# Kernel optimization log

Measured on AMD Instinct MI355X. Metric: run time of the kernel, lower is better.

Reference implementation:

```python
import jax, jax.numpy as jnp
import numpy as np

B, S, H = 8, 2048, 512
M = 4096
TEMP = 0.1
EPS = 1e-6


def setup_inputs() -> dict:
    key = jax.random.key(0)
    ks = jax.random.split(key, 8)
    scale = 1.0 / np.sqrt(H)
    return {
        "hidden_states": jax.random.normal(ks[0], (B, S, H), dtype=jnp.float32),
        "memory_keys": jax.random.normal(ks[1], (M, H), dtype=jnp.float32),
        "memory_values": jax.random.normal(ks[2], (M, H), dtype=jnp.float32),
        "Wk": jax.random.normal(ks[3], (H, H), dtype=jnp.float32) * scale,
        "bk": jnp.zeros((H,), dtype=jnp.float32),
        "Wo": jax.random.normal(ks[4], (H, H), dtype=jnp.float32) * scale,
        "bo": jnp.zeros((H,), dtype=jnp.float32),
        "memory_usage": jax.random.randint(ks[5], (M,), 0, 2, dtype=jnp.int32),
    }


def reference(hidden_states, memory_keys, memory_values, Wk, bk, Wo, bo, memory_usage):
    # key projection: [B,S,H]
    q = jnp.einsum("bsh,kh->bsk", hidden_states, Wk) + bk
    # L2-style normalization with eps inside rsqrt (matches torch.rsqrt(norm_sq + 1e-6))
    q_n = q * jax.lax.rsqrt(jnp.sum(q * q, axis=-1, keepdims=True) + EPS)
    mk_n = memory_keys * jax.lax.rsqrt(
        jnp.sum(memory_keys * memory_keys, axis=-1, keepdims=True) + EPS
    )
    # cosine-similarity scores over the memory bank: [B,S,M]
    scores = jnp.einsum("bsk,mk->bsm", q_n, mk_n) / TEMP
    mask = (memory_usage > 0).astype(scores.dtype)  # [M]
    scores = scores * mask + (-1e9) * (1.0 - mask)
    attn = jax.nn.softmax(scores, axis=-1)  # [B,S,M]
    retrieved = jnp.einsum("bsm,mv->bsv", attn, memory_values)  # [B,S,H]
    out = jnp.einsum("bsv,hv->bsh", retrieved, Wo) + bo
    return out
```

## Files before the change

kernel.cpp:

```cpp
#include <hip/hip_runtime.h>
#include <cstdint>
#include <cstddef>

#define H_DIM   512
#define M_DIM   4096

typedef unsigned short u16;
typedef short bf16x8 __attribute__((ext_vector_type(8)));
typedef float f32x4  __attribute__((ext_vector_type(4)));

__device__ __forceinline__ u16 f2b(float f) {
  union { float f; uint32_t u; } v; v.f = f;
  uint32_t u = v.u + (0x7FFFu + ((v.u >> 16) & 1u));
  return (u16)(u >> 16);
}

__global__ void k_f2bf(const float* __restrict__ in, u16* __restrict__ out, int n4) {
  int i = blockIdx.x * blockDim.x + threadIdx.x;
  if (i < n4) {
    float4 v = ((const float4*)in)[i];
    ushort4 o;
    o.x = f2b(v.x); o.y = f2b(v.y); o.z = f2b(v.z); o.w = f2b(v.w);
    ((ushort4*)out)[i] = o;
  }
}

__global__ void k_f2bf_ww(const float* __restrict__ wk, const float* __restrict__ wo,
                          u16* __restrict__ owk, u16* __restrict__ owo) {
  int i = blockIdx.x * blockDim.x + threadIdx.x;
  const float* src = (i < 65536) ? wk : wo;
  u16* dst = (i < 65536) ? owk : owo;
  int j = i & 65535;
  float4 v = ((const float4*)src)[j];
  ushort4 o;
  o.x = f2b(v.x); o.y = f2b(v.y); o.z = f2b(v.z); o.w = f2b(v.w);
  ((ushort4*)dst)[j] = o;
}

__global__ void k_compact(const int* __restrict__ usage, int* __restrict__ idx,
                          int* __restrict__ meta) {
  __shared__ int cnt[256];
  int t = threadIdx.x;
  int base = t * 16;
  int c = 0;
  #pragma unroll
  for (int i = 0; i < 16; ++i) c += (usage[base + i] > 0) ? 1 : 0;
  cnt[t] = c;
  __syncthreads();
  for (int d = 1; d < 256; d <<= 1) {
    int v = (t >= d) ? cnt[t - d] : 0;
    __syncthreads();
    cnt[t] += v;
    __syncthreads();
  }
  int pos = cnt[t] - c;
  for (int i = 0; i < 16; ++i)
    if (usage[base + i] > 0) idx[pos++] = base + i;
  if (t == 0) {
    int total = cnt[255];
    int keff = ((total + 127) >> 7) << 7;
    meta[0] = total; meta[1] = keff; meta[2] = keff >> 5; meta[3] = keff >> 7;
  }
}

__global__ void k_gather_both(const float* __restrict__ keys, const float* __restrict__ vals,
                              const int* __restrict__ idx, const int* __restrict__ meta,
                              u16* __restrict__ okeys, u16* __restrict__ ovals) {
  int j    = blockIdx.x * 4 + (threadIdx.x >> 6);
  int lane = threadIdx.x & 63;
  int count = meta[0];
  ushort4* kp = (ushort4*)(okeys + (size_t)j * H_DIM);
  ushort4* vp = (ushort4*)(ovals + (size_t)j * H_DIM);
  if (j >= count) {
    ushort4 z = {0, 0, 0, 0};
    kp[lane] = z; kp[lane + 64] = z;
    vp[lane] = z; vp[lane + 64] = z;
    return;
  }
  int src = idx[j];
  const float4* rp = (const float4*)(keys + (size_t)src * H_DIM);
  float4 a = rp[lane];
  float4 b = rp[lane + 64];
  float ss = a.x*a.x + a.y*a.y + a.z*a.z + a.w*a.w
           + b.x*b.x + b.y*b.y + b.z*b.z + b.w*b.w;
  #pragma unroll
  for (int d = 1; d < 64; d <<= 1) ss += __shfl_xor(ss, d, 64);
  float s = rsqrtf(ss + 1e-6f);
  ushort4 oa, ob;
  oa.x = f2b(a.x*s); oa.y = f2b(a.y*s); oa.z = f2b(a.z*s); oa.w = f2b(a.w*s);
  ob.x = f2b(b.x*s); ob.y = f2b(b.y*s); ob.z = f2b(b.z*s); ob.w = f2b(b.w*s);
  kp[lane]      = oa;
  kp[lane + 64] = ob;
  const float4* vr = (const float4*)(vals + (size_t)src * H_DIM);
  float4 c0 = vr[lane];
  float4 c1 = vr[lane + 64];
  ushort4 va, vb;
  va.x = f2b(c0.x); va.y = f2b(c0.y); va.z = f2b(c0.z); va.w = f2b(c0.w);
  vb.x = f2b(c1.x); vb.y = f2b(c1.y); vb.z = f2b(c1.z); vb.w = f2b(c1.w);
  vp[lane]      = va;
  vp[lane + 64] = vb;
}

__global__ void k_rsq(const float* __restrict__ qss, float* __restrict__ rsq) {
  int r = blockIdx.x * blockDim.x + threadIdx.x;
  float s = 0.0f;
  #pragma unroll
  for (int i = 0; i < 8; ++i) s += qss[(size_t)r * 8 + i];
  rsq[r] = rsqrtf(s + 1e-6f);
}

__global__ void k_reduce_l(const float* __restrict__ lpart, float* __restrict__ linv,
                           const int* __restrict__ meta) {
  int r = blockIdx.x * blockDim.x + threadIdx.x;
  int n = meta[1] >> 6;
  float s = 0.0f;
  for (int i = 0; i < n; ++i) s += lpart[(size_t)r * 64 + i];
  linv[r] = 1.0f / s;
}

#define EPI_QPROJ 0
#define EPI_MW    1
#define EPI_P     2
#define EPI_OUT   3

template<int EPI>
__global__ __launch_bounds__(256, 3)
void k_gemm_bt(const u16* __restrict__ A, const u16* __restrict__ B,
               int N, int K,
               const int* __restrict__ meta,
               float* __restrict__ outf, u16* __restrict__ outh,
               const float* __restrict__ bias,
               float* __restrict__ aux,
               const float* __restrict__ rowscale) {
  __shared__ u16 Ah[2][128 * 32];
  __shared__ u16 Bh[2][128 * 32];

  const int tid  = threadIdx.x;
  const int wave = tid >> 6, lane = tid & 63;
  const int wr = (wave >> 1) * 64;
  const int wc = (wave & 1) * 64;

  int t0, t_end, t_step, kel, fixedb;
  if (EPI == EPI_QPROJ) {
    fixedb = blockIdx.x; t0 = blockIdx.y; t_end = t0 + 1; t_step = 1; kel = K;
  } else if (EPI == EPI_MW) {
    fixedb = blockIdx.y; t0 = blockIdx.x; t_end = meta[1] >> 7; t_step = 16; kel = K;
  } else if (EPI == EPI_P) {
    int id = blockIdx.x + (blockIdx.y << 4);
    int xcd = id & 7, s = id >> 3;
    fixedb = xcd * 16 + (s >> 4);
    t0 = s & 15;
    t_end = meta[1] >> 7; t_step = 16; kel = K;
  } else {
    int id = blockIdx.x + (blockIdx.y << 2);
    int xcd = id & 7, s = id >> 3;
    fixedb = xcd * 16 + (s >> 2);
    t0 = s & 3; t_end = t0 + 1; t_step = 1; kel = meta[1];
  }
  const int kiters = kel >> 5;

  const int srow   = lane & 15;
  const int schunk = lane >> 4;
  const int lds_off = schunk * 128 + srow * 8;

  const int fr = lane & 15;
  const int fbase = (lane >> 4) * 128 + fr * 8;
  const int g = lane >> 4;

  const char* Ac = (const char*)A;
  const char* Bc = (const char*)B;

  for (int t = t0; t < t_end; t += t_step) {
    const int row0 = ((EPI == EPI_P) ? t : fixedb) << 7;
    const int col0 = ((EPI == EPI_P) ? fixedb : t) << 7;
    __syncthreads();

    uint32_t aB[2], bB[2];
    #pragma unroll
    for (int s2 = 0; s2 < 2; ++s2) {
      aB[s2] = (uint32_t)(((size_t)(row0 + (wave + s2 * 4) * 16 + srow) * (size_t)K
                           + (size_t)(schunk * 8)) * 2u);
      bB[s2] = (uint32_t)(((size_t)(col0 + (wave + s2 * 4) * 16 + srow) * (size_t)K
                           + (size_t)(schunk * 8)) * 2u);
    }

    f32x4 acc[4][4];
    const f32x4 z = {0.0f, 0.0f, 0.0f, 0.0f};
    #pragma unroll
    for (int i = 0; i < 4; ++i)
      #pragma unroll
      for (int j = 0; j < 4; ++j) acc[i][j] = z;

    bf16x8 rA[2], rB[2];
    auto gload = [&](int k0) {
      const uint32_t kb = (uint32_t)(k0 << 1);
      #pragma unroll
      for (int s2 = 0; s2 < 2; ++s2) rA[s2] = *(const bf16x8*)(Ac + aB[s2] + kb);
      #pragma unroll
      for (int s2 = 0; s2 < 2; ++s2) rB[s2] = *(const bf16x8*)(Bc + bB[s2] + kb);
    };

    gload(0);
    for (int it = 0; it < kiters; ++it) {
      const int cur = it & 1;
      #pragma unroll
      for (int s2 = 0; s2 < 2; ++s2)
        *(bf16x8*)&Ah[cur][(wave + s2 * 4) * 512 + lds_off] = rA[s2];
      #pragma unroll
      for (int s2 = 0; s2 < 2; ++s2)
        *(bf16x8*)&Bh[cur][(wave + s2 * 4) * 512 + lds_off] = rB[s2];
      if (it + 1 < kiters) gload((it + 1) << 5);
      __syncthreads();

      bf16x8 af[4], bfv[4];
      #pragma unroll
      for (int i = 0; i < 4; ++i)
        af[i] = *(const bf16x8*)&Ah[cur][((wr >> 4) + i) * 512 + fbase];
      #pragma unroll
      for (int j = 0; j < 4; ++j)
        bfv[j] = *(const bf16x8*)&Bh[cur][((wc >> 4) + j) * 512 + fbase];
      #pragma unroll
      for (int i = 0; i < 4; ++i)
        #pragma unroll
        for (int j = 0; j < 4; ++j)
          acc[i][j] = __builtin_amdgcn_mfma_f32_16x16x32_bf16(af[i], bfv[j], acc[i][j], 0, 0, 0);
    }

    if (EPI == EPI_QPROJ) {
      float sj[4] = {0.f, 0.f, 0.f, 0.f};
      #pragma unroll
      for (int i = 0; i < 4; ++i) {
        const int kb = row0 + wr + i * 16 + g * 4;
        const float4 bkv = *(const float4*)(bias + kb);
        #pragma unroll
        for (int j = 0; j < 4; ++j) {
          const size_t rcol = (size_t)(col0 + wc + j * 16 + fr);
          float v0 = acc[i][j][0] + bkv.x;
          float v1 = acc[i][j][1] + bkv.y;
          float v2 = acc[i][j][2] + bkv.z;
          float v3 = acc[i][j][3] + bkv.w;
          ushort4 st; st.x = f2b(v0); st.y = f2b(v1); st.z = f2b(v2); st.w = f2b(v3);
          *(ushort4*)(outh + rcol * H_DIM + kb) = st;
          sj[j] += v0 * v0 + v1 * v1 + v2 * v2 + v3 * v3;
        }
      }
      const int slot = (row0 + wr) >> 6;
      #pragma unroll
      for (int j = 0; j < 4; ++j) {
        float s = sj[j];
        s += __shfl_xor(s, 16, 64);
        s += __shfl_xor(s, 32, 64);
        if (lane < 16)
          aux[(size_t)(col0 + wc + j * 16 + lane) * 8 + slot] = s;
      }
    } else if (EPI == EPI_MW) {
      #pragma unroll
      for (int i = 0; i < 4; ++i) {
        #pragma unroll
        for (int r = 0; r < 4; ++r) {
          int grow = row0 + wr + i * 16 + g * 4 + r;
          #pragma unroll
          for (int j = 0; j < 4; ++j) {
            int gcol = col0 + wc + j * 16 + fr;
            outh[(size_t)grow * (size_t)N + gcol] = f2b(acc[i][j][r]);
          }
        }
      }
    } else if (EPI == EPI_P) {
      const int count = meta[0];
      float rq10[4];
      #pragma unroll
      for (int j = 0; j < 4; ++j)
        rq10[j] = rowscale[col0 + wc + j * 16 + fr] * 10.0f;
      float sj[4] = {0.f, 0.f, 0.f, 0.f};
      #pragma unroll
      for (int i = 0; i < 4; ++i) {
        const int mb = row0 + wr + i * 16 + g * 4;
        #pragma unroll
        for (int j = 0; j < 4; ++j) {
          const size_t rcol = (size_t)(col0 + wc + j * 16 + fr);
          float p0 = (mb + 0 < count) ? __expf(acc[i][j][0] * rq10[j]) : 0.0f;
          float p1 = (mb + 1 < count) ? __expf(acc[i][j][1] * rq10[j]) : 0.0f;
          float p2 = (mb + 2 < count) ? __expf(acc[i][j][2] * rq10[j]) : 0.0f;
          float p3 = (mb + 3 < count) ? __expf(acc[i][j][3] * rq10[j]) : 0.0f;
          ushort4 st; st.x = f2b(p0); st.y = f2b(p1); st.z = f2b(p2); st.w = f2b(p3);
          *(ushort4*)(outh + rcol * M_DIM + mb) = st;
          sj[j] += (p0 + p1) + (p2 + p3);
        }
      }
      const int slot = (row0 + wr) >> 6;
      #pragma unroll
      for (int j = 0; j < 4; ++j) {
        float s = sj[j];
        s += __shfl_xor(s, 16, 64);
        s += __shfl_xor(s, 32, 64);
        if (lane < 16)
          aux[(size_t)(col0 + wc + j * 16 + lane) * 64 + slot] = s;
      }
    } else {
      float bv[4];
      #pragma unroll
      for (int j = 0; j < 4; ++j) bv[j] = bias[col0 + wc + j * 16 + fr];
      #pragma unroll
      for (int i = 0; i < 4; ++i) {
        #pragma unroll
        for (int r = 0; r < 4; ++r) {
          int grow = row0 + wr + i * 16 + g * 4 + r;
          float sc = rowscale[grow];
          #pragma unroll
          for (int j = 0; j < 4; ++j) {
            int gcol = col0 + wc + j * 16 + fr;
            outf[(size_t)grow * (size_t)N + gcol] = acc[i][j][r] * sc + bv[j];
          }
        }
      }
    }
  }
}

extern "C" void kernel_launch(void* const* d_in, const int* in_sizes, int n_in,
                              void* d_out, int out_size, void* d_ws, size_t ws_size,
                              hipStream_t stream) {
  const float* hidden = (const float*)d_in[0];
  const float* mkeys  = (const float*)d_in[1];
  const float* mvals  = (const float*)d_in[2];
  const float* Wk     = (const float*)d_in[3];
  const float* bk     = (const float*)d_in[4];
  const float* Wo     = (const float*)d_in[5];
  const float* bo     = (const float*)d_in[6];
  const int*   usage  = (const int*)d_in[7];
  (void)in_sizes; (void)n_in; (void)out_size; (void)ws_size;

  char* ws = (char*)d_ws;
  u16*   hb    = (u16*)(ws + 0);
  int*   idx   = (int*)(ws + 0);
  int*   meta  = (int*)(ws + 16384);
  float* lpart = (float*)(ws + 1048576);
  u16*   wkb   = (u16*)(ws + 16777216);
  u16*   wob   = (u16*)(ws + 17301504);
  u16*   mkn   = (u16*)(ws + 17825792);
  u16*   mv_c  = (u16*)(ws + 22020096);
  u16*   qb    = (u16*)(ws + 26214400);
  u16*   MWt   = (u16*)(ws + 42991616);
  u16*   P     = (u16*)(ws + 47185920);
  float* qss   = (float*)(ws + 47185920);
  float* rsqQ  = (float*)(ws + 181665792);
  float* linv  = (float*)(ws + 183828480);

  k_f2bf<<<8192, 256, 0, stream>>>(hidden, hb, 2097152);
  k_f2bf_ww<<<512, 256, 0, stream>>>(Wk, Wo, wkb, wob);

  k_gemm_bt<EPI_QPROJ><<<dim3(4, 128), 256, 0, stream>>>(wkb, hb, 512, 512,
      nullptr, nullptr, qb, bk, qss, nullptr);
  k_rsq<<<64, 256, 0, stream>>>(qss, rsqQ);

  k_compact<<<1, 256, 0, stream>>>(usage, idx, meta);
  k_gather_both<<<1024, 256, 0, stream>>>(mkeys, mvals, idx, meta, mkn, mv_c);

  k_gemm_bt<EPI_MW><<<dim3(16, 4), 256, 0, stream>>>(wob, mv_c, M_DIM, 512,
      meta, nullptr, MWt, nullptr, nullptr, nullptr);

  k_gemm_bt<EPI_P><<<dim3(16, 128), 256, 0, stream>>>(mkn, qb, M_DIM, 512,
      meta, nullptr, P, nullptr, lpart, rsqQ);
  k_reduce_l<<<64, 256, 0, stream>>>(lpart, linv, meta);

  k_gemm_bt<EPI_OUT><<<dim3(4, 128), 256, 0, stream>>>(P, MWt, 512, M_DIM,
      meta, (float*)d_out, nullptr, bo, nullptr, linv);
}
```

Measured before the change: 292.4 us.

## Use larger 256-wide tiles with 512-thread blocks for the two big GEMMs

Adds a new GEMM kernel with 512-thread blocks and 256x256 (scores) or 128x256 (output) tiles, and uses it for the score/exp GEMM and the final output GEMM. Each tile reuses operands more per LDS load and needs fewer blocks. The output GEMM swaps operand roles so it writes float4 rows with a vectorized bias add. The score kernel exits early on tiles beyond the compacted memory count and zeros the adjacent partial-sum slot. Larger tiles raise register and LDS use per block and may lower occupancy.

```diff
diff --git a/kernel.cpp b/kernel.cpp
--- a/kernel.cpp
+++ b/kernel.cpp
@@ -120,8 +120,6 @@
 
 #define EPI_QPROJ 0
 #define EPI_MW    1
-#define EPI_P     2
-#define EPI_OUT   3
 
 template<int EPI>
 __global__ __launch_bounds__(256, 3)
@@ -143,19 +141,8 @@
   int t0, t_end, t_step, kel, fixedb;
   if (EPI == EPI_QPROJ) {
     fixedb = blockIdx.x; t0 = blockIdx.y; t_end = t0 + 1; t_step = 1; kel = K;
-  } else if (EPI == EPI_MW) {
+  } else {
     fixedb = blockIdx.y; t0 = blockIdx.x; t_end = meta[1] >> 7; t_step = 16; kel = K;
-  } else if (EPI == EPI_P) {
-    int id = blockIdx.x + (blockIdx.y << 4);
-    int xcd = id & 7, s = id >> 3;
-    fixedb = xcd * 16 + (s >> 4);
-    t0 = s & 15;
-    t_end = meta[1] >> 7; t_step = 16; kel = K;
-  } else {
-    int id = blockIdx.x + (blockIdx.y << 2);
-    int xcd = id & 7, s = id >> 3;
-    fixedb = xcd * 16 + (s >> 2);
-    t0 = s & 3; t_end = t0 + 1; t_step = 1; kel = meta[1];
   }
   const int kiters = kel >> 5;
 
@@ -171,8 +158,8 @@
   const char* Bc = (const char*)B;
 
   for (int t = t0; t < t_end; t += t_step) {
-    const int row0 = ((EPI == EPI_P) ? t : fixedb) << 7;
-    const int col0 = ((EPI == EPI_P) ? fixedb : t) << 7;
+    const int row0 = fixedb << 7;
+    const int col0 = t << 7;
     __syncthreads();
 
     uint32_t aB[2], bB[2];
@@ -253,7 +240,7 @@
         if (lane < 16)
           aux[(size_t)(col0 + wc + j * 16 + lane) * 8 + slot] = s;
       }
-    } else if (EPI == EPI_MW) {
+    } else {
       #pragma unroll
       for (int i = 0; i < 4; ++i) {
         #pragma unroll
@@ -266,53 +253,168 @@
           }
         }
       }
-    } else if (EPI == EPI_P) {
-      const int count = meta[0];
-      float rq10[4];
-      #pragma unroll
-      for (int j = 0; j < 4; ++j)
-        rq10[j] = rowscale[col0 + wc + j * 16 + fr] * 10.0f;
-      float sj[4] = {0.f, 0.f, 0.f, 0.f};
-      #pragma unroll
-      for (int i = 0; i < 4; ++i) {
-        const int mb = row0 + wr + i * 16 + g * 4;
-        #pragma unroll
-        for (int j = 0; j < 4; ++j) {
-          const size_t rcol = (size_t)(col0 + wc + j * 16 + fr);
-          float p0 = (mb + 0 < count) ? __expf(acc[i][j][0] * rq10[j]) : 0.0f;
-          float p1 = (mb + 1 < count) ? __expf(acc[i][j][1] * rq10[j]) : 0.0f;
-          float p2 = (mb + 2 < count) ? __expf(acc[i][j][2] * rq10[j]) : 0.0f;
-          float p3 = (mb + 3 < count) ? __expf(acc[i][j][3] * rq10[j]) : 0.0f;
-          ushort4 st; st.x = f2b(p0); st.y = f2b(p1); st.z = f2b(p2); st.w = f2b(p3);
-          *(ushort4*)(outh + rcol * M_DIM + mb) = st;
-          sj[j] += (p0 + p1) + (p2 + p3);
-        }
-      }
-      const int slot = (row0 + wr) >> 6;
-      #pragma unroll
-      for (int j = 0; j < 4; ++j) {
-        float s = sj[j];
-        s += __shfl_xor(s, 16, 64);
-        s += __shfl_xor(s, 32, 64);
-        if (lane < 16)
-          aux[(size_t)(col0 + wc + j * 16 + lane) * 64 + slot] = s;
-      }
-    } else {
-      float bv[4];
-      #pragma unroll
-      for (int j = 0; j < 4; ++j) bv[j] = bias[col0 + wc + j * 16 + fr];
-      #pragma unroll
-      for (int i = 0; i < 4; ++i) {
-        #pragma unroll
-        for (int r = 0; r < 4; ++r) {
-          int grow = row0 + wr + i * 16 + g * 4 + r;
-          float sc = rowscale[grow];
-          #pragma unroll
-          for (int j = 0; j < 4; ++j) {
-            int gcol = col0 + wc + j * 16 + fr;
-            outf[(size_t)grow * (size_t)N + gcol] = acc[i][j][r] * sc + bv[j];
-          }
-        }
+    }
+  }
+}
+
+#define EPI2_P   0
+#define EPI2_OUT 1
+
+template<int EPI>
+__global__ __launch_bounds__(512, 2)
+void k_gemm2(const u16* __restrict__ A, const u16* __restrict__ B,
+             const int* __restrict__ meta,
+             float* __restrict__ outf, u16* __restrict__ outh,
+             const float* __restrict__ bias,
+             float* __restrict__ aux,
+             const float* __restrict__ rowscale) {
+  constexpr int BM  = (EPI == EPI2_P) ? 256 : 128;
+  constexpr int MF  = BM / 32;
+  constexpr int NF  = 4;
+  constexpr int NLA = BM / 128;
+  constexpr int NLB = 2;
+
+  __shared__ u16 Ah[2][BM * 32];
+  __shared__ u16 Bh[2][256 * 32];
+
+  const int tid  = threadIdx.x;
+  const int wave = tid >> 6, lane = tid & 63;
+  const int wave_m = wave >> 2, wave_n = wave & 3;
+  const int wm0 = wave_m * (BM >> 1);
+  const int wn0 = wave_n * 64;
+  const int fr  = lane & 15, g = lane >> 4;
+  const int fbase = g * 128 + fr * 8;
+
+  int m0, r0, kel;
+  if (EPI == EPI2_P) {
+    int id = blockIdx.x + (blockIdx.y << 4);
+    int xcd = id & 7, s = id >> 3;
+    r0 = (xcd * 8 + (s >> 4)) << 8;
+    m0 = (s & 15) << 8;
+    if (m0 >= meta[1]) return;
+    kel = 512;
+  } else {
+    int id = blockIdx.x + (blockIdx.y << 2);
+    int xcd = id & 7, s = id >> 3;
+    r0 = (xcd * 8 + (s >> 2)) << 8;
+    m0 = (s & 3) << 7;
+    kel = meta[1];
+  }
+  const int kiters = kel >> 5;
+  const int kstr = (EPI == EPI2_P) ? 512 : M_DIM;
+
+  const char* Ac = (const char*)A;
+  const char* Bc = (const char*)B;
+  uint32_t aB[NLA], bB[NLB];
+  #pragma unroll
+  for (int s2 = 0; s2 < NLA; ++s2) {
+    int unit = tid + s2 * 512;
+    int row = ((unit >> 6) << 4) + (unit & 15);
+    int kch = (unit >> 4) & 3;
+    aB[s2] = (uint32_t)(((size_t)(m0 + row) * (size_t)kstr + (size_t)(kch * 8)) * 2u);
+  }
+  #pragma unroll
+  for (int s2 = 0; s2 < NLB; ++s2) {
+    int unit = tid + s2 * 512;
+    int row = ((unit >> 6) << 4) + (unit & 15);
+    int kch = (unit >> 4) & 3;
+    bB[s2] = (uint32_t)(((size_t)(r0 + row) * (size_t)kstr + (size_t)(kch * 8)) * 2u);
+  }
+
+  f32x4 acc[MF][NF];
+  const f32x4 z = {0.0f, 0.0f, 0.0f, 0.0f};
+  #pragma unroll
+  for (int i = 0; i < MF; ++i)
+    #pragma unroll
+    for (int j = 0; j < NF; ++j) acc[i][j] = z;
+
+  bf16x8 rA[NLA], rB[NLB];
+  auto gload = [&](int k0) {
+    const uint32_t kb = (uint32_t)(k0 << 1);
+    #pragma unroll
+    for (int s2 = 0; s2 < NLA; ++s2) rA[s2] = *(const bf16x8*)(Ac + aB[s2] + kb);
+    #pragma unroll
+    for (int s2 = 0; s2 < NLB; ++s2) rB[s2] = *(const bf16x8*)(Bc + bB[s2] + kb);
+  };
+
+  gload(0);
+  for (int it = 0; it < kiters; ++it) {
+    const int cur = it & 1;
+    #pragma unroll
+    for (int s2 = 0; s2 < NLA; ++s2)
+      *(bf16x8*)&Ah[cur][(tid + s2 * 512) * 8] = rA[s2];
+    #pragma unroll
+    for (int s2 = 0; s2 < NLB; ++s2)
+      *(bf16x8*)&Bh[cur][(tid + s2 * 512) * 8] = rB[s2];
+    if (it + 1 < kiters) gload((it + 1) << 5);
+    __syncthreads();
+
+    bf16x8 af[MF], bfv[NF];
+    #pragma unroll
+    for (int i = 0; i < MF; ++i)
+      af[i] = *(const bf16x8*)&Ah[cur][((wm0 >> 4) + i) * 512 + fbase];
+    #pragma unroll
+    for (int j = 0; j < NF; ++j)
+      bfv[j] = *(const bf16x8*)&Bh[cur][((wn0 >> 4) + j) * 512 + fbase];
+    #pragma unroll
+    for (int i = 0; i < MF; ++i)
+      #pragma unroll
+      for (int j = 0; j < NF; ++j)
+        acc[i][j] = __builtin_amdgcn_mfma_f32_16x16x32_bf16(af[i], bfv[j], acc[i][j], 0, 0, 0);
+  }
+
+  if (EPI == EPI2_P) {
+    const int count = meta[0];
+    float rq10[NF];
+    #pragma unroll
+    for (int j = 0; j < NF; ++j)
+      rq10[j] = rowscale[r0 + wn0 + j * 16 + fr] * 10.0f;
+    float sj[NF] = {0.f, 0.f, 0.f, 0.f};
+    #pragma unroll
+    for (int i = 0; i < MF; ++i) {
+      const int mb = m0 + wm0 + i * 16 + g * 4;
+      #pragma unroll
+      for (int j = 0; j < NF; ++j) {
+        const size_t rr = (size_t)(r0 + wn0 + j * 16 + fr);
+        float p0 = (mb + 0 < count) ? __expf(acc[i][j][0] * rq10[j]) : 0.0f;
+        float p1 = (mb + 1 < count) ? __expf(acc[i][j][1] * rq10[j]) : 0.0f;
+        float p2 = (mb + 2 < count) ? __expf(acc[i][j][2] * rq10[j]) : 0.0f;
+        float p3 = (mb + 3 < count) ? __expf(acc[i][j][3] * rq10[j]) : 0.0f;
+        ushort4 st; st.x = f2b(p0); st.y = f2b(p1); st.z = f2b(p2); st.w = f2b(p3);
+        *(ushort4*)(outh + rr * M_DIM + mb) = st;
+        sj[j] += (p0 + p1) + (p2 + p3);
+      }
+    }
+    const int slot = (m0 + wm0) >> 6;
+    #pragma unroll
+    for (int j = 0; j < NF; ++j) {
+      float s = sj[j];
+      s += __shfl_xor(s, 16, 64);
+      s += __shfl_xor(s, 32, 64);
+      if (lane < 16) {
+        const size_t rr = (size_t)(r0 + wn0 + j * 16 + lane);
+        aux[rr * 64 + slot]     = s;
+        aux[rr * 64 + slot + 1] = 0.0f;
+      }
+    }
+  } else {
+    float scl[NF];
+    #pragma unroll
+    for (int j = 0; j < NF; ++j)
+      scl[j] = rowscale[r0 + wn0 + j * 16 + fr];
+    #pragma unroll
+    for (int i = 0; i < MF; ++i) {
+      const int hb = m0 + wm0 + i * 16 + g * 4;
+      const float4 bv = *(const float4*)(bias + hb);
+      #pragma unroll
+      for (int j = 0; j < NF; ++j) {
+        const size_t rr = (size_t)(r0 + wn0 + j * 16 + fr);
+        float4 o;
+        o.x = acc[i][j][0] * scl[j] + bv.x;
+        o.y = acc[i][j][1] * scl[j] + bv.y;
+        o.z = acc[i][j][2] * scl[j] + bv.z;
+        o.w = acc[i][j][3] * scl[j] + bv.w;
+        *(float4*)(outf + rr * H_DIM + hb) = o;
       }
     }
   }
@@ -360,10 +462,10 @@
   k_gemm_bt<EPI_MW><<<dim3(16, 4), 256, 0, stream>>>(wob, mv_c, M_DIM, 512,
       meta, nullptr, MWt, nullptr, nullptr, nullptr);
 
-  k_gemm_bt<EPI_P><<<dim3(16, 128), 256, 0, stream>>>(mkn, qb, M_DIM, 512,
-      meta, nullptr, P, nullptr, lpart, rsqQ);
+  k_gemm2<EPI2_P><<<dim3(16, 64), 512, 0, stream>>>(mkn, qb, meta,
+      nullptr, P, nullptr, lpart, rsqQ);
   k_reduce_l<<<64, 256, 0, stream>>>(lpart, linv, meta);
 
-  k_gemm_bt<EPI_OUT><<<dim3(4, 128), 256, 0, stream>>>(P, MWt, 512, M_DIM,
-      meta, (float*)d_out, nullptr, bo, nullptr, linv);
-}
+  k_gemm2<EPI2_OUT><<<dim3(4, 64), 512, 0, stream>>>(MWt, P, meta,
+      (float*)d_out, nullptr, bo, nullptr, linv);
+}
```

After: 255.1 us. 12.8% less time.
